# Kernel tuning notes

Measured on AMD Instinct MI355X. Metric: run time of the kernel, lower is better.

## Reference

```python
import jax, jax.numpy as jnp
import numpy as np

N = 100000   # nodes
E = 1600000  # edges (avg in-degree 16)
D = 64       # feature dim (dim_in = dim_out)


def setup_inputs() -> dict:
    key = jax.random.key(0)
    k1, k2, k3, k4, k5, k6 = jax.random.split(key, 6)
    h = jax.random.normal(k1, (N, D), dtype=jnp.float32)
    src = jax.random.randint(k2, (E,), 0, N, dtype=jnp.int32)
    dst = jax.random.randint(k3, (E,), 0, N, dtype=jnp.int32)
    scale = 1.0 / np.sqrt(D).astype(np.float32)
    W1 = jax.random.normal(k4, (D, D), dtype=jnp.float32) * scale  # Linear(dim_in, dim_out, bias=False)
    W2 = jax.random.normal(k5, (D, D), dtype=jnp.float32) * scale  # Linear(dim_out, dim_out, bias=True)
    b2 = jax.random.normal(k6, (D,), dtype=jnp.float32) * scale
    return {"h": h, "src": src, "dst": dst, "W1": W1, "W2": W2, "b2": b2}


def reference(h, src, dst, W1, W2, b2):
    # GINConv with 'max' aggregation, eps = 0 (DGL default, not learned):
    #   out = MLP( h + max_{(u->v) in E} h[u] )
    msgs = h[src]  # [E, D] gather of source features
    agg = jax.ops.segment_max(msgs, dst, num_segments=N)  # [N, D]
    # Nodes with no in-edges: DGL's max-reduce yields zeros, segment_max yields -inf.
    deg = jax.ops.segment_sum(jnp.ones((E,), dtype=h.dtype), dst, num_segments=N)  # [N]
    agg = jnp.where(deg[:, None] > 0, agg, jnp.zeros((), dtype=h.dtype))
    x = h + agg                       # (1 + eps) * h_dst + agg, eps = 0
    y = jnp.maximum(x @ W1.T, 0.0)    # Linear(no bias) + ReLU
    return y @ W2.T + b2              # Linear(bias)
```

## Files before the change

kernel.cpp:

```cpp
#include <hip/hip_runtime.h>
#include <math.h>

#define NN 100000
#define EE 1600000
#define D 64

#define CSH 9
#define CSIZE 512
#define NCB 196
#define CAPC 8800
#define GCS 16
#define BSH 7
#define BSIZE 128
#define NBUK 782
#define AST 65

#define EPB 2048
#define NCHUNK ((EE + EPB - 1) / EPB)
#define KPER (EPB / 256)
#define GRID 1024


__device__ __forceinline__ unsigned short encbf(float x) {
    unsigned int b = __float_as_uint(x);
    unsigned short u = (unsigned short)((b + 0x7FFFu + ((b >> 16) & 1u)) >> 16);
    return u ^ ((u & 0x8000u) ? 0xFFFFu : 0x8000u);
}

__device__ __forceinline__ unsigned int pkmax(unsigned int a, unsigned int b) {
    unsigned int d;
    asm("v_pk_max_u16 %0, %1, %2" : "=v"(d) : "v"(a), "v"(b));
    return d;
}

__global__ void __launch_bounds__(256) kAP2(const float* __restrict__ h,
                                            unsigned short* __restrict__ hb,
                                            const float* __restrict__ W1, float* __restrict__ W1T,
                                            const float* __restrict__ W2, float* __restrict__ W2T,
                                            const int* __restrict__ src, const int* __restrict__ dst,
                                            int* __restrict__ gcurC, int* __restrict__ bdataC) {
    __shared__ int lcnt[NCB];
    __shared__ int lofs[NCB];
    __shared__ int gb[NCB];
    __shared__ int lcur2[NCB];
    __shared__ unsigned int ent[EPB];
    __shared__ unsigned char bkb[EPB];
    const int t = threadIdx.x;
    const int b = blockIdx.x;

    if (b < NCHUNK) {
        for (int i = t; i < NCB; i += 256) lcnt[i] = 0;
        __syncthreads();
        const int e0 = b * EPB;
        int es[KPER], ed[KPER];
#pragma unroll
        for (int k = 0; k < KPER; k++) {
            int e = e0 + k * 256 + t;
            int d = -1, s = 0;
            if (e < EE) {
                d = dst[e];
                s = src[e];
                atomicAdd(&lcnt[d >> CSH], 1);
            }
            ed[k] = d; es[k] = s;
        }
        __syncthreads();
        if (t < NCB) lofs[t] = lcnt[t];
        __syncthreads();
        for (int s = 1; s < NCB; s <<= 1) {
            int v = 0;
            if (t < NCB) { v = lofs[t]; if (t >= s) v += lofs[t - s]; }
            __syncthreads();
            if (t < NCB) lofs[t] = v;
            __syncthreads();
        }
        if (t < NCB) {
            int c = lcnt[t];
            int ex = lofs[t] - c;
            lcur2[t] = ex;
            lofs[t] = ex;
            gb[t] = c ? atomicAdd(&gcurC[t * GCS], c) : 0;
        }
        __syncthreads();
#pragma unroll
        for (int k = 0; k < KPER; k++) {
            if (ed[k] >= 0) {
                int bk = ed[k] >> CSH;
                int p = atomicAdd(&lcur2[bk], 1);
                ent[p] = ((unsigned)es[k] << CSH) | (unsigned)(ed[k] & (CSIZE - 1));
                bkb[p] = (unsigned char)bk;
            }
        }
        __syncthreads();
        const int tot = (e0 + EPB <= EE) ? EPB : (EE - e0);
        for (int i = t; i < tot; i += 256) {
            int bk = bkb[i];
            int p = gb[bk] + (i - lofs[bk]);
            if (p < CAPC) bdataC[bk * CAPC + p] = (int)ent[i];
        }
    }

    const int gid = b * 256 + t;
    const int gsz = gridDim.x * 256;
    const float4* h4 = (const float4*)h;
    ushort4* hb4 = (ushort4*)hb;
    for (int idx = gid; idx < NN * D / 4; idx += gsz) {
        float4 v = h4[idx];
        ushort4 r;
        r.x = encbf(v.x); r.y = encbf(v.y); r.z = encbf(v.z); r.w = encbf(v.w);
        hb4[idx] = r;
    }
    if (gid < D * D) {
        int k = gid >> 6, j = gid & 63;
        W1T[gid] = W1[j * D + k];
        W2T[gid] = W2[j * D + k];
    }
}

__global__ void __launch_bounds__(512) kC3(const float* __restrict__ h,
                                           const unsigned short* __restrict__ hb,
                                           const int* __restrict__ gcurC,
                                           const int* __restrict__ bdataC,
                                           const float* __restrict__ W1T,
                                           const float* __restrict__ W2T,
                                           const float* __restrict__ b2,
                                           float* __restrict__ out) {
    __shared__ unsigned int acc[BSIZE * AST];
    __shared__ int deg[BSIZE];
    __shared__ int scn[BSIZE];
    __shared__ int cur[BSIZE];
    float* fac = (float*)acc;
    unsigned int* elist = acc;
    const int t = threadIdx.x;
    const int b = blockIdx.x;
    const int cb = b >> 2;
    const unsigned int sub = (unsigned)(b & 3);
    int cnt = gcurC[cb * GCS];
    if (cnt > CAPC) cnt = CAPC;
    const int cbase = cb * CAPC;

    if (t < BSIZE) deg[t] = 0;
    __syncthreads();
    for (int i = t; i < cnt; i += 512) {
        unsigned int e = (unsigned)bdataC[cbase + i];
        if (((e >> BSH) & 3u) == sub) atomicAdd(&deg[e & (BSIZE - 1)], 1);
    }
    __syncthreads();
    if (t < BSIZE) scn[t] = deg[t];
    __syncthreads();
    for (int s = 1; s < BSIZE; s <<= 1) {
        int v = 0;
        if (t < BSIZE) { v = scn[t]; if (t >= s) v += scn[t - s]; }
        __syncthreads();
        if (t < BSIZE) scn[t] = v;
        __syncthreads();
    }
    if (t < BSIZE) cur[t] = scn[t] - deg[t];
    __syncthreads();
    for (int i = t; i < cnt; i += 512) {
        unsigned int e = (unsigned)bdataC[cbase + i];
        if (((e >> BSH) & 3u) == sub) {
            int pos = atomicAdd(&cur[e & (BSIZE - 1)], 1);
            elist[pos] = e >> CSH;
        }
    }
    __syncthreads();

    const int wave = t >> 6, lane = t & 63;
    const int oct = lane >> 3;
    const int fbyte = (lane & 7) * 16;
    const char* hbB = (const char*)hb;
    unsigned int m[2][4];
#pragma unroll
    for (int p = 0; p < 2; ++p)
#pragma unroll
        for (int c = 0; c < 4; ++c) m[p][c] = 0u;

#pragma unroll
    for (int p = 0; p < 2; ++p) {
        const int n8 = wave * 16 + p * 8 + oct;
        const int dg = deg[n8];
        const int ofs = scn[n8] - dg;
        int md = dg;
        md = max(md, __shfl_xor(md, 8));
        md = max(md, __shfl_xor(md, 16));
        md = max(md, __shfl_xor(md, 32));
        for (int r0 = 0; r0 < md; r0 += 8) {
            uint4 u[8];
#pragma unroll
            for (int g = 0; g < 8; ++g) {
                int r = r0 + g;
                u[g] = make_uint4(0u, 0u, 0u, 0u);
                if (r < dg) {
                    unsigned int sidx = elist[ofs + r];
                    u[g] = *(const uint4*)(hbB + (size_t)sidx * 128 + fbyte);
                }
            }
#pragma unroll
            for (int g = 0; g < 8; ++g) {
                m[p][0] = pkmax(m[p][0], u[g].x);
                m[p][1] = pkmax(m[p][1], u[g].y);
                m[p][2] = pkmax(m[p][2], u[g].z);
                m[p][3] = pkmax(m[p][3], u[g].w);
            }
        }
    }
    __syncthreads();

#pragma unroll
    for (int p = 0; p < 2; ++p) {
        const int n8 = wave * 16 + p * 8 + oct;
        const int v = b * BSIZE + n8;
        const int f0 = (lane & 7) * 8;
        float x[8];
#pragma unroll
        for (int c = 0; c < 4; ++c) {
            unsigned int w = m[p][c];
            unsigned int klo = w & 0xFFFFu;
            unsigned int khi = w >> 16;
            float mlo = 0.0f, mhi = 0.0f;
            if (klo) {
                unsigned int bb = (klo & 0x8000u) ? (klo ^ 0x8000u) : ((~klo) & 0xFFFFu);
                mlo = __uint_as_float(bb << 16);
            }
            if (khi) {
                unsigned int bb = (khi & 0x8000u) ? (khi ^ 0x8000u) : ((~khi) & 0xFFFFu);
                mhi = __uint_as_float(bb << 16);
            }
            x[2 * c] = mlo;
            x[2 * c + 1] = mhi;
        }
        if (v < NN) {
            const float4* hp = (const float4*)(h + (size_t)v * D + f0);
            float4 a0 = hp[0], a1 = hp[1];
            x[0] += a0.x; x[1] += a0.y; x[2] += a0.z; x[3] += a0.w;
            x[4] += a1.x; x[5] += a1.y; x[6] += a1.z; x[7] += a1.w;
        } else {
#pragma unroll
            for (int j = 0; j < 8; ++j) x[j] = 0.0f;
        }
#pragma unroll
        for (int j = 0; j < 8; ++j) fac[n8 * AST + f0 + j] = x[j];
    }
    __syncthreads();

    const int n = t & (BSIZE - 1);
    const int hq = __builtin_amdgcn_readfirstlane(t >> 7);
    const float* w1 = W1T + hq * 16;
    const float* w2 = W2T + hq * 16;
    float y[16];
#pragma unroll
    for (int jj = 0; jj < 16; jj++) y[jj] = 0.0f;
#pragma unroll 8
    for (int k = 0; k < D; k++) {
        float xk = fac[n * AST + k];
#pragma unroll
        for (int jj = 0; jj < 16; jj++)
            y[jj] = fmaf(xk, w1[k * D + jj], y[jj]);
    }
#pragma unroll
    for (int jj = 0; jj < 16; jj++) y[jj] = fmaxf(y[jj], 0.0f);
    __syncthreads();
#pragma unroll
    for (int jj = 0; jj < 16; jj++) fac[n * AST + hq * 16 + jj] = y[jj];
    __syncthreads();

    float o[16];
#pragma unroll
    for (int ii = 0; ii < 16; ii++) o[ii] = b2[hq * 16 + ii];
#pragma unroll 8
    for (int j = 0; j < D; j++) {
        float yj = fac[n * AST + j];
#pragma unroll
        for (int ii = 0; ii < 16; ii++)
            o[ii] = fmaf(yj, w2[j * D + ii], o[ii]);
    }
    int v = b * BSIZE + n;
    if (v < NN) {
        float4* op = (float4*)(out + (size_t)v * D + hq * 16);
#pragma unroll
        for (int c = 0; c < 4; c++)
            op[c] = make_float4(o[4 * c], o[4 * c + 1], o[4 * c + 2], o[4 * c + 3]);
    }
}

extern "C" void kernel_launch(void* const* d_in, const int* in_sizes, int n_in,
                              void* d_out, int out_size, void* d_ws, size_t ws_size,
                              hipStream_t stream) {
    const float* h   = (const float*)d_in[0];
    const int*   src = (const int*)d_in[1];
    const int*   dst = (const int*)d_in[2];
    const float* W1  = (const float*)d_in[3];
    const float* W2  = (const float*)d_in[4];
    const float* b2  = (const float*)d_in[5];
    float* out = (float*)d_out;

    int* ws = (int*)d_ws;
    int* gcurC  = ws;
    int* bdataC = ws + NCB * GCS;
    float* W1T = (float*)(ws + NCB * GCS + NCB * CAPC);
    float* W2T = W1T + D * D;
    unsigned short* hb = (unsigned short*)(W2T + D * D);

    hipMemsetAsync(gcurC, 0, NCB * GCS * sizeof(int), stream);
    kAP2<<<GRID, 256, 0, stream>>>(h, hb, W1, W1T, W2, W2T, src, dst, gcurC, bdataC);
    kC3<<<NBUK, 512, 0, stream>>>(h, hb, gcurC, bdataC, W1T, W2T, b2, out);
}
```

Before: 180.7 us.

## Split each coarse bucket across eight 64-node blocks with XCD-aware block mapping

The aggregate+MLP kernel now uses 256-thread blocks covering 64 destination nodes, so each 512-node coarse chunk is handled by eight blocks instead of four. Block indices are remapped so that blocks sharing a coarse chunk fall on the same residue mod 8, which likely places them on the same XCD and lets them share the chunk's edge list in L2. This doubles parallelism and lowers per-block LDS, at the cost of every block rescanning the whole chunk edge list, which now doubles total scan work, plus some early-exit blocks.

Result: faster. 175.0 us (-3.2%).

```diff
diff --git a/kernel.cpp b/kernel.cpp
--- a/kernel.cpp
+++ b/kernel.cpp
@@ -10,10 +10,11 @@
 #define NCB 196
 #define CAPC 8800
 #define GCS 16
-#define BSH 7
-#define BSIZE 128
-#define NBUK 782
-#define AST 65
+#define BSH2 6
+#define BSIZE2 64
+#define NBUK2 1563
+#define AST2 65
+#define CGRID2 1600
 
 #define EPB 2048
 #define NCHUNK ((EE + EPB - 1) / EPB)
@@ -117,7 +118,7 @@
     }
 }
 
-__global__ void __launch_bounds__(512) kC3(const float* __restrict__ h,
+__global__ void __launch_bounds__(256) kC4(const float* __restrict__ h,
                                            const unsigned short* __restrict__ hb,
                                            const int* __restrict__ gcurC,
                                            const int* __restrict__ bdataC,
@@ -125,42 +126,47 @@
                                            const float* __restrict__ W2T,
                                            const float* __restrict__ b2,
                                            float* __restrict__ out) {
-    __shared__ unsigned int acc[BSIZE * AST];
-    __shared__ int deg[BSIZE];
-    __shared__ int scn[BSIZE];
-    __shared__ int cur[BSIZE];
+    const int i = blockIdx.x;
+    const int x = i & 7, m = i >> 3;
+    const int j = m % 25, r = m / 25;
+    const int c = x + 8 * j;
+    if (c >= NCB) return;
+    const int b = c * 8 + r;
+    if (b >= NBUK2) return;
+
+    __shared__ unsigned int acc[BSIZE2 * AST2];
+    __shared__ int deg[BSIZE2];
+    __shared__ int scn[BSIZE2];
+    __shared__ int cur[BSIZE2];
     float* fac = (float*)acc;
     unsigned int* elist = acc;
     const int t = threadIdx.x;
-    const int b = blockIdx.x;
-    const int cb = b >> 2;
-    const unsigned int sub = (unsigned)(b & 3);
-    int cnt = gcurC[cb * GCS];
+    int cnt = gcurC[c * GCS];
     if (cnt > CAPC) cnt = CAPC;
-    const int cbase = cb * CAPC;
-
-    if (t < BSIZE) deg[t] = 0;
-    __syncthreads();
-    for (int i = t; i < cnt; i += 512) {
-        unsigned int e = (unsigned)bdataC[cbase + i];
-        if (((e >> BSH) & 3u) == sub) atomicAdd(&deg[e & (BSIZE - 1)], 1);
-    }
-    __syncthreads();
-    if (t < BSIZE) scn[t] = deg[t];
-    __syncthreads();
-    for (int s = 1; s < BSIZE; s <<= 1) {
+    const int cbase = c * CAPC;
+
+    if (t < BSIZE2) deg[t] = 0;
+    __syncthreads();
+    for (int i2 = t; i2 < cnt; i2 += 256) {
+        unsigned int e = (unsigned)bdataC[cbase + i2];
+        if (((e >> BSH2) & 7u) == (unsigned)r) atomicAdd(&deg[e & (BSIZE2 - 1)], 1);
+    }
+    __syncthreads();
+    if (t < BSIZE2) scn[t] = deg[t];
+    __syncthreads();
+    for (int s = 1; s < BSIZE2; s <<= 1) {
         int v = 0;
-        if (t < BSIZE) { v = scn[t]; if (t >= s) v += scn[t - s]; }
-        __syncthreads();
-        if (t < BSIZE) scn[t] = v;
-        __syncthreads();
-    }
-    if (t < BSIZE) cur[t] = scn[t] - deg[t];
-    __syncthreads();
-    for (int i = t; i < cnt; i += 512) {
-        unsigned int e = (unsigned)bdataC[cbase + i];
-        if (((e >> BSH) & 3u) == sub) {
-            int pos = atomicAdd(&cur[e & (BSIZE - 1)], 1);
+        if (t < BSIZE2) { v = scn[t]; if (t >= s) v += scn[t - s]; }
+        __syncthreads();
+        if (t < BSIZE2) scn[t] = v;
+        __syncthreads();
+    }
+    if (t < BSIZE2) cur[t] = scn[t] - deg[t];
+    __syncthreads();
+    for (int i2 = t; i2 < cnt; i2 += 256) {
+        unsigned int e = (unsigned)bdataC[cbase + i2];
+        if (((e >> BSH2) & 7u) == (unsigned)r) {
+            int pos = atomicAdd(&cur[e & (BSIZE2 - 1)], 1);
             elist[pos] = e >> CSH;
         }
     }
@@ -170,11 +176,11 @@
     const int oct = lane >> 3;
     const int fbyte = (lane & 7) * 16;
     const char* hbB = (const char*)hb;
-    unsigned int m[2][4];
+    unsigned int mm[2][4];
 #pragma unroll
     for (int p = 0; p < 2; ++p)
 #pragma unroll
-        for (int c = 0; c < 4; ++c) m[p][c] = 0u;
+        for (int cc = 0; cc < 4; ++cc) mm[p][cc] = 0u;
 
 #pragma unroll
     for (int p = 0; p < 2; ++p) {
@@ -189,19 +195,19 @@
             uint4 u[8];
 #pragma unroll
             for (int g = 0; g < 8; ++g) {
-                int r = r0 + g;
+                int rr = r0 + g;
                 u[g] = make_uint4(0u, 0u, 0u, 0u);
-                if (r < dg) {
-                    unsigned int sidx = elist[ofs + r];
+                if (rr < dg) {
+                    unsigned int sidx = elist[ofs + rr];
                     u[g] = *(const uint4*)(hbB + (size_t)sidx * 128 + fbyte);
                 }
             }
 #pragma unroll
             for (int g = 0; g < 8; ++g) {
-                m[p][0] = pkmax(m[p][0], u[g].x);
-                m[p][1] = pkmax(m[p][1], u[g].y);
-                m[p][2] = pkmax(m[p][2], u[g].z);
-                m[p][3] = pkmax(m[p][3], u[g].w);
+                mm[p][0] = pkmax(mm[p][0], u[g].x);
+                mm[p][1] = pkmax(mm[p][1], u[g].y);
+                mm[p][2] = pkmax(mm[p][2], u[g].z);
+                mm[p][3] = pkmax(mm[p][3], u[g].w);
             }
         }
     }
@@ -210,12 +216,12 @@
 #pragma unroll
     for (int p = 0; p < 2; ++p) {
         const int n8 = wave * 16 + p * 8 + oct;
-        const int v = b * BSIZE + n8;
+        const int v = b * BSIZE2 + n8;
         const int f0 = (lane & 7) * 8;
-        float x[8];
-#pragma unroll
-        for (int c = 0; c < 4; ++c) {
-            unsigned int w = m[p][c];
+        float xx[8];
+#pragma unroll
+        for (int cc = 0; cc < 4; ++cc) {
+            unsigned int w = mm[p][cc];
             unsigned int klo = w & 0xFFFFu;
             unsigned int khi = w >> 16;
             float mlo = 0.0f, mhi = 0.0f;
@@ -227,25 +233,25 @@
                 unsigned int bb = (khi & 0x8000u) ? (khi ^ 0x8000u) : ((~khi) & 0xFFFFu);
                 mhi = __uint_as_float(bb << 16);
             }
-            x[2 * c] = mlo;
-            x[2 * c + 1] = mhi;
+            xx[2 * cc] = mlo;
+            xx[2 * cc + 1] = mhi;
         }
         if (v < NN) {
             const float4* hp = (const float4*)(h + (size_t)v * D + f0);
             float4 a0 = hp[0], a1 = hp[1];
-            x[0] += a0.x; x[1] += a0.y; x[2] += a0.z; x[3] += a0.w;
-            x[4] += a1.x; x[5] += a1.y; x[6] += a1.z; x[7] += a1.w;
+            xx[0] += a0.x; xx[1] += a0.y; xx[2] += a0.z; xx[3] += a0.w;
+            xx[4] += a1.x; xx[5] += a1.y; xx[6] += a1.z; xx[7] += a1.w;
         } else {
 #pragma unroll
-            for (int j = 0; j < 8; ++j) x[j] = 0.0f;
-        }
-#pragma unroll
-        for (int j = 0; j < 8; ++j) fac[n8 * AST + f0 + j] = x[j];
-    }
-    __syncthreads();
-
-    const int n = t & (BSIZE - 1);
-    const int hq = __builtin_amdgcn_readfirstlane(t >> 7);
+            for (int jj = 0; jj < 8; ++jj) xx[jj] = 0.0f;
+        }
+#pragma unroll
+        for (int jj = 0; jj < 8; ++jj) fac[n8 * AST2 + f0 + jj] = xx[jj];
+    }
+    __syncthreads();
+
+    const int n = t & (BSIZE2 - 1);
+    const int hq = __builtin_amdgcn_readfirstlane(t >> 6);
     const float* w1 = W1T + hq * 16;
     const float* w2 = W2T + hq * 16;
     float y[16];
@@ -253,7 +259,7 @@
     for (int jj = 0; jj < 16; jj++) y[jj] = 0.0f;
 #pragma unroll 8
     for (int k = 0; k < D; k++) {
-        float xk = fac[n * AST + k];
+        float xk = fac[n * AST2 + k];
 #pragma unroll
         for (int jj = 0; jj < 16; jj++)
             y[jj] = fmaf(xk, w1[k * D + jj], y[jj]);
@@ -262,25 +268,25 @@
     for (int jj = 0; jj < 16; jj++) y[jj] = fmaxf(y[jj], 0.0f);
     __syncthreads();
 #pragma unroll
-    for (int jj = 0; jj < 16; jj++) fac[n * AST + hq * 16 + jj] = y[jj];
+    for (int jj = 0; jj < 16; jj++) fac[n * AST2 + hq * 16 + jj] = y[jj];
     __syncthreads();
 
     float o[16];
 #pragma unroll
     for (int ii = 0; ii < 16; ii++) o[ii] = b2[hq * 16 + ii];
 #pragma unroll 8
-    for (int j = 0; j < D; j++) {
-        float yj = fac[n * AST + j];
+    for (int jj = 0; jj < D; jj++) {
+        float yj = fac[n * AST2 + jj];
 #pragma unroll
         for (int ii = 0; ii < 16; ii++)
-            o[ii] = fmaf(yj, w2[j * D + ii], o[ii]);
-    }
-    int v = b * BSIZE + n;
+            o[ii] = fmaf(yj, w2[jj * D + ii], o[ii]);
+    }
+    int v = b * BSIZE2 + n;
     if (v < NN) {
         float4* op = (float4*)(out + (size_t)v * D + hq * 16);
 #pragma unroll
-        for (int c = 0; c < 4; c++)
-            op[c] = make_float4(o[4 * c], o[4 * c + 1], o[4 * c + 2], o[4 * c + 3]);
+        for (int cc = 0; cc < 4; cc++)
+            op[cc] = make_float4(o[4 * cc], o[4 * cc + 1], o[4 * cc + 2], o[4 * cc + 3]);
     }
 }
 
@@ -304,5 +310,5 @@
 
     hipMemsetAsync(gcurC, 0, NCB * GCS * sizeof(int), stream);
     kAP2<<<GRID, 256, 0, stream>>>(h, hb, W1, W1T, W2, W2T, src, dst, gcurC, bdataC);
-    kC3<<<NBUK, 512, 0, stream>>>(h, hb, gcurC, bdataC, W1T, W2T, b2, out);
-}
+    kC4<<<CGRID2, 256, 0, stream>>>(h, hb, gcurC, bdataC, W1T, W2T, b2, out);
+}
```
